# Kernel tuning notes

Measured on AMD Instinct MI355X. Metric: run time of the kernel, lower is better.

## Reference

```python
import jax, jax.numpy as jnp
import numpy as np

B, S, D, H, L, MAXSEQ = 32, 512, 768, 1024, 4, 1024


def setup_inputs() -> dict:
    key = jax.random.key(0)
    ks = jax.random.split(key, 10)
    s_in = 1.0 / np.sqrt(H)
    inp = {
        "x": jax.random.normal(ks[0], (B, S, D), dtype=jnp.float32),
        "pos_emb": jax.random.normal(ks[1], (1, MAXSEQ, D), dtype=jnp.float32),
        # layer 0 input->hidden weights (GRU: 3 gates stacked)
        "W_ih0": jax.random.uniform(ks[2], (3 * H, D), jnp.float32, -s_in, s_in),
        # layers 1..L-1 input->hidden weights
        "W_ih": jax.random.uniform(ks[3], (L - 1, 3 * H, H), jnp.float32, -s_in, s_in),
        "W_hh": jax.random.uniform(ks[4], (L, 3 * H, H), jnp.float32, -s_in, s_in),
        "b_ih": jax.random.uniform(ks[5], (L, 3 * H), jnp.float32, -s_in, s_in),
        "b_hh": jax.random.uniform(ks[6], (L, 3 * H), jnp.float32, -s_in, s_in),
        "W_out": jax.random.uniform(ks[7], (D, H), jnp.float32, -s_in, s_in),
        "b_out": jax.random.uniform(ks[8], (D,), jnp.float32, -s_in, s_in),
    }
    return inp


def _gru_cell(x, h, Wih, Whh, bih, bhh):
    # torch.nn.GRUCell math; gates stacked [r, z, n]
    gi = x @ Wih.T + bih  # [B, 3H]
    gh = h @ Whh.T + bhh  # [B, 3H]
    i_r, i_z, i_n = jnp.split(gi, 3, axis=-1)
    h_r, h_z, h_n = jnp.split(gh, 3, axis=-1)
    r = jax.nn.sigmoid(i_r + h_r)
    z = jax.nn.sigmoid(i_z + h_z)
    n = jnp.tanh(i_n + r * h_n)
    return (1.0 - z) * n + z * h


def reference(x, pos_emb, W_ih0, W_ih, W_hh, b_ih, b_hh, W_out, b_out):
    b, s, _ = x.shape
    xp = x + pos_emb[:, :s, :]          # add positional embedding
    xs = jnp.swapaxes(xp, 0, 1)         # [S, B, D] for scan over time

    def step(hs, xt):                   # hs: [L, B, H]
        inp = xt
        new_hs = []
        for l in range(L):
            Wih = W_ih0 if l == 0 else W_ih[l - 1]
            h = _gru_cell(inp, hs[l], Wih, W_hh[l], b_ih[l], b_hh[l])
            new_hs.append(h)
            inp = h
        return jnp.stack(new_hs), inp

    h0 = jnp.zeros((L, b, H), dtype=x.dtype)
    hs_final, outs = jax.lax.scan(step, h0, xs)  # outs: [S, B, H]
    out_seq = jnp.swapaxes(outs, 0, 1) @ W_out.T + b_out  # [B, S, D]
    return out_seq, hs_final
```

## Files before the change

kernel.cpp:

```cpp
#include <hip/hip_runtime.h>

#define B_ 32
#define S_ 512
#define D_ 768
#define H_ 1024
#define L_ 4
#define TH 3072
#define NPL 64
#define NITER (S_ + L_ - 1)

typedef unsigned short u16;
typedef unsigned int u32;
typedef __bf16 bf16x8 __attribute__((ext_vector_type(8)));
typedef float f32x4 __attribute__((ext_vector_type(4)));

__device__ __forceinline__ u16 f2b(float f) {
  unsigned u = __builtin_bit_cast(unsigned, f);
  u += 0x7fffu + ((u >> 16) & 1u);
  return (u16)(u >> 16);
}
__device__ __forceinline__ float b2f(u16 h) {
  return __builtin_bit_cast(float, ((unsigned)h) << 16);
}
__device__ __forceinline__ unsigned pack2(float a, float b) {
  return (unsigned)f2b(a) | ((unsigned)f2b(b) << 16);
}

__global__ __launch_bounds__(256) void cvt_kernel(const float* __restrict__ src,
                                                  u16* __restrict__ dst, int n4) {
  int i = blockIdx.x * 256 + threadIdx.x;
  int stride = gridDim.x * 256;
  for (; i < n4; i += stride) {
    float4 f = ((const float4*)src)[i];
    uint2 o;
    o.x = pack2(f.x, f.y);
    o.y = pack2(f.z, f.w);
    ((uint2*)dst)[i] = o;
  }
}

__global__ __launch_bounds__(256) void gi0_gemm(const float* __restrict__ x,
                                                const float* __restrict__ pos,
                                                const u16* __restrict__ W0,
                                                const float* __restrict__ bih0,
                                                u16* __restrict__ GI0) {
  const int n0 = blockIdx.x * 64;
  const int m0 = blockIdx.y * 64;
  __shared__ u16 sA[64 * 72];
  __shared__ u16 sB[64 * 72];
  const int tid = threadIdx.x, lane = tid & 63, wid = tid >> 6;
  const int wm = wid >> 1, wn = wid & 1;
  const int fr = lane & 15, fk = (lane >> 4) * 8;
  f32x4 acc[2][2] = {};
  for (int k0 = 0; k0 < D_; k0 += 64) {
    for (int sl = tid; sl < 512; sl += 256) {
      int r = sl >> 3, c = sl & 7;
      int m = m0 + r, si = m >> 5, b = m & 31;
      const float* xp = x + (size_t)((b << 9) + si) * D_ + k0 + c * 8;
      const float* pp = pos + (size_t)si * D_ + k0 + c * 8;
      float4 x0 = *(const float4*)xp, x1 = *(const float4*)(xp + 4);
      float4 p0 = *(const float4*)pp, p1 = *(const float4*)(pp + 4);
      uint4 o;
      o.x = pack2(x0.x + p0.x, x0.y + p0.y);
      o.y = pack2(x0.z + p0.z, x0.w + p0.w);
      o.z = pack2(x1.x + p1.x, x1.y + p1.y);
      o.w = pack2(x1.z + p1.z, x1.w + p1.w);
      *(uint4*)&sA[r * 72 + c * 8] = o;
      *(uint4*)&sB[r * 72 + c * 8] =
          *(const uint4*)(W0 + (size_t)(n0 + r) * D_ + k0 + c * 8);
    }
    __syncthreads();
#pragma unroll
    for (int kk = 0; kk < 2; ++kk) {
      bf16x8 a0 = *(const bf16x8*)&sA[(wm * 32 + fr) * 72 + kk * 32 + fk];
      bf16x8 a1 = *(const bf16x8*)&sA[(wm * 32 + 16 + fr) * 72 + kk * 32 + fk];
      bf16x8 b0 = *(const bf16x8*)&sB[(wn * 32 + fr) * 72 + kk * 32 + fk];
      bf16x8 b1 = *(const bf16x8*)&sB[(wn * 32 + 16 + fr) * 72 + kk * 32 + fk];
      acc[0][0] = __builtin_amdgcn_mfma_f32_16x16x32_bf16(a0, b0, acc[0][0], 0, 0, 0);
      acc[0][1] = __builtin_amdgcn_mfma_f32_16x16x32_bf16(a0, b1, acc[0][1], 0, 0, 0);
      acc[1][0] = __builtin_amdgcn_mfma_f32_16x16x32_bf16(a1, b0, acc[1][0], 0, 0, 0);
      acc[1][1] = __builtin_amdgcn_mfma_f32_16x16x32_bf16(a1, b1, acc[1][1], 0, 0, 0);
    }
    __syncthreads();
  }
#pragma unroll
  for (int mi = 0; mi < 2; ++mi)
#pragma unroll
    for (int ni = 0; ni < 2; ++ni)
#pragma unroll
      for (int r = 0; r < 4; ++r) {
        int m = m0 + wm * 32 + mi * 16 + (lane >> 4) * 4 + r;
        int n = n0 + wn * 32 + ni * 16 + fr;
        GI0[(size_t)m * TH + n] = f2b(acc[mi][ni][r] + bih0[n]);
      }
}

__global__ __launch_bounds__(256) void out_gemm(const u16* __restrict__ H3,
                                                const u16* __restrict__ Wo,
                                                const float* __restrict__ bo,
                                                float* __restrict__ out) {
  const int n0 = blockIdx.x * 64;
  const int m0 = blockIdx.y * 64;
  __shared__ u16 sA[64 * 72];
  __shared__ u16 sB[64 * 72];
  const int tid = threadIdx.x, lane = tid & 63, wid = tid >> 6;
  const int wm = wid >> 1, wn = wid & 1;
  const int fr = lane & 15, fk = (lane >> 4) * 8;
  f32x4 acc[2][2] = {};
  for (int k0 = 0; k0 < H_; k0 += 64) {
    for (int sl = tid; sl < 512; sl += 256) {
      int r = sl >> 3, c = sl & 7;
      int m = m0 + r, b = m >> 9, si = m & 511;
      *(uint4*)&sA[r * 72 + c * 8] =
          *(const uint4*)(H3 + (size_t)((si << 5) + b) * H_ + k0 + c * 8);
      *(uint4*)&sB[r * 72 + c * 8] =
          *(const uint4*)(Wo + (size_t)(n0 + r) * H_ + k0 + c * 8);
    }
    __syncthreads();
#pragma unroll
    for (int kk = 0; kk < 2; ++kk) {
      bf16x8 a0 = *(const bf16x8*)&sA[(wm * 32 + fr) * 72 + kk * 32 + fk];
      bf16x8 a1 = *(const bf16x8*)&sA[(wm * 32 + 16 + fr) * 72 + kk * 32 + fk];
      bf16x8 b0 = *(const bf16x8*)&sB[(wn * 32 + fr) * 72 + kk * 32 + fk];
      bf16x8 b1 = *(const bf16x8*)&sB[(wn * 32 + 16 + fr) * 72 + kk * 32 + fk];
      acc[0][0] = __builtin_amdgcn_mfma_f32_16x16x32_bf16(a0, b0, acc[0][0], 0, 0, 0);
      acc[0][1] = __builtin_amdgcn_mfma_f32_16x16x32_bf16(a0, b1, acc[0][1], 0, 0, 0);
      acc[1][0] = __builtin_amdgcn_mfma_f32_16x16x32_bf16(a1, b0, acc[1][0], 0, 0, 0);
      acc[1][1] = __builtin_amdgcn_mfma_f32_16x16x32_bf16(a1, b1, acc[1][1], 0, 0, 0);
    }
    __syncthreads();
  }
#pragma unroll
  for (int mi = 0; mi < 2; ++mi)
#pragma unroll
    for (int ni = 0; ni < 2; ++ni)
#pragma unroll
      for (int r = 0; r < 4; ++r) {
        int m = m0 + wm * 32 + mi * 16 + (lane >> 4) * 4 + r;
        int n = n0 + wn * 32 + ni * 16 + fr;
        out[(size_t)m * D_ + n] = acc[mi][ni][r] + bo[n];
      }
}

__global__ __launch_bounds__(512, 1) void rnn_persist(
    const u16* __restrict__ Whh, const u16* __restrict__ Wih,
    const u16* __restrict__ GI0, const float* __restrict__ bih,
    const float* __restrict__ bhh, u16* __restrict__ hg ,
    int* flags , u16* __restrict__ H3, float* __restrict__ hsf) {
  const int bid = blockIdx.x;
  const int l = bid >> 6;
  const int n0 = (bid & 63) << 4;
  const int tid = threadIdx.x, lane = tid & 63, wid = tid >> 6;
  const int fr = lane & 15, q = lane >> 4;

  __shared__ float red[8][3][32][20];

  bf16x8 w[3][8];
  if (l == 0) {
    const int kb = wid << 7;
#pragma unroll
    for (int g = 0; g < 3; ++g)
#pragma unroll
      for (int kt = 0; kt < 4; ++kt) {
        const u16* p = Whh + (((size_t)((g << 10) + n0 + fr)) << 10) + kb +
                       kt * 32 + q * 8;
        asm volatile("global_load_dwordx4 %0, %1, off"
                     : "=v"(w[g][kt]) : "v"(p));
      }
  } else {
    const int mat = wid >> 2;
    const u16* Wp = (mat == 0) ? (Wih + (((size_t)(l - 1) * TH) << 10))
                               : (Whh + (((size_t)l * TH) << 10));
    const int kb = (wid & 3) << 8;
#pragma unroll
    for (int g = 0; g < 3; ++g)
#pragma unroll
      for (int kt = 0; kt < 8; ++kt) {
        const u16* p = Wp + (((size_t)((g << 10) + n0 + fr)) << 10) + kb +
                       kt * 32 + q * 8;
        asm volatile("global_load_dwordx4 %0, %1, off"
                     : "=v"(w[g][kt]) : "v"(p));
      }
  }
  asm volatile("s_waitcnt vmcnt(0)" ::: "memory");

  const int* pw;
  if (l == 0) {
    pw = flags + ((0 << 6) + (wid << 3) + (lane & 7)) * 16;
  } else {
    const int srcl = (wid < 4) ? (l - 1) : l;
    pw = flags + ((srcl << 6) + ((wid & 3) << 4) + (lane & 15)) * 16;
  }
  const int* f_p1 = (l < 3) ? flags + (((l + 1) << 6) + lane) * 16
                            : flags + ((l << 6) + lane) * 16;
  int* f_mine = flags + ((l << 6) + (bid & 63)) * 16;

  const int gb = tid >> 4;
  const int jj = tid & 15;
  const int gj = n0 + jj;
  float bihv[3], bhhv[3];
#pragma unroll
  for (int g = 0; g < 3; ++g) {
    bihv[g] = (l > 0) ? bih[l * TH + (g << 10) + gj] : 0.f;
    bhhv[g] = bhh[l * TH + (g << 10) + gj];
  }
  float hpriv = 0.f;
  __syncthreads();

  for (int s = 0; s < NITER; ++s) {
    const int t = s - l;
    if (t < 0 || t >= S_) {
      if (tid == 0) {
        int v = s + 1;
        asm volatile("global_store_dword %0, %1, off sc0 sc1" ::"v"(f_mine), "v"(v)
                     : "memory");
      }
      continue;
    }
    const int prev = (s - 1) & 3;

    float gp0 = 0.f, gp1 = 0.f, gp2 = 0.f;
    if (l == 0) {
      const u16* gp = GI0 + (size_t)((t << 5) + gb) * TH + gj;
      gp0 = b2f(gp[0]);
      gp1 = b2f(gp[1024]);
      gp2 = b2f(gp[2048]);
    }

    for (;;) {
      int fv;
      asm volatile("global_load_dword %0, %1, off sc0 sc1\n\ts_waitcnt vmcnt(0)"
                   : "=v"(fv) : "v"(pw) : "memory");
      __builtin_amdgcn_sched_barrier(0);
      if (__all(fv >= s)) break;
      __builtin_amdgcn_s_sleep(1);
    }

    f32x4 acc[2][3] = {};
    if (l == 0) {
      const u16* hp = hg + (prev << 15);
      const int kb = wid << 7;
      bf16x8 afr[2][4];
#pragma unroll
      for (int mt = 0; mt < 2; ++mt)
#pragma unroll
        for (int kt = 0; kt < 4; ++kt) {
          const u16* p = hp + (((mt << 4) + fr) << 10) + kb + kt * 32 + q * 8;
          asm volatile("global_load_dwordx4 %0, %1, off sc0 sc1"
                       : "=v"(afr[mt][kt]) : "v"(p) : "memory");
        }
      asm volatile("s_waitcnt vmcnt(0)" ::: "memory");
      __builtin_amdgcn_sched_barrier(0);
#pragma unroll
      for (int kt = 0; kt < 4; ++kt)
#pragma unroll
        for (int g = 0; g < 3; ++g) {
          acc[0][g] = __builtin_amdgcn_mfma_f32_16x16x32_bf16(afr[0][kt], w[g][kt], acc[0][g], 0, 0, 0);
          acc[1][g] = __builtin_amdgcn_mfma_f32_16x16x32_bf16(afr[1][kt], w[g][kt], acc[1][g], 0, 0, 0);
        }
    } else {
      const u16* hsrc = (wid < 4) ? (hg + ((((l - 1) << 2) | prev) << 15))
                                  : (hg + (((l << 2) | prev) << 15));
      const int kb = (wid & 3) << 8;
      bf16x8 afr[2][8];
#pragma unroll
      for (int mt = 0; mt < 2; ++mt)
#pragma unroll
        for (int kt = 0; kt < 8; ++kt) {
          const u16* p = hsrc + (((mt << 4) + fr) << 10) + kb + kt * 32 + q * 8;
          asm volatile("global_load_dwordx4 %0, %1, off sc0 sc1"
                       : "=v"(afr[mt][kt]) : "v"(p) : "memory");
        }
      asm volatile("s_waitcnt vmcnt(0)" ::: "memory");
      __builtin_amdgcn_sched_barrier(0);
#pragma unroll
      for (int kt = 0; kt < 8; ++kt)
#pragma unroll
        for (int g = 0; g < 3; ++g) {
          acc[0][g] = __builtin_amdgcn_mfma_f32_16x16x32_bf16(afr[0][kt], w[g][kt], acc[0][g], 0, 0, 0);
          acc[1][g] = __builtin_amdgcn_mfma_f32_16x16x32_bf16(afr[1][kt], w[g][kt], acc[1][g], 0, 0, 0);
        }
    }

#pragma unroll
    for (int mt = 0; mt < 2; ++mt)
#pragma unroll
      for (int g = 0; g < 3; ++g)
#pragma unroll
        for (int r = 0; r < 4; ++r)
          red[wid][g][(mt << 4) + q * 4 + r][fr] = acc[mt][g][r];

    if (wid == 7) {
      const int thr = s - 2;
      for (;;) {
        int fv;
        asm volatile("global_load_dword %0, %1, off sc0 sc1\n\ts_waitcnt vmcnt(0)"
                     : "=v"(fv) : "v"(f_p1) : "memory");
        __builtin_amdgcn_sched_barrier(0);
        if (__all(fv >= thr)) break;
        __builtin_amdgcn_s_sleep(1);
      }
    }
    __syncthreads();

    float gi[3], gh[3];
#pragma unroll
    for (int g = 0; g < 3; ++g) {
      float s0 = red[0][g][gb][jj] + red[1][g][gb][jj];
      float s1 = red[2][g][gb][jj] + red[3][g][gb][jj];
      float s2 = red[4][g][gb][jj] + red[5][g][gb][jj];
      float s3 = red[6][g][gb][jj] + red[7][g][gb][jj];
      if (l == 0) {
        gh[g] = s0 + s1 + s2 + s3 + bhhv[g];
      } else {
        gi[g] = s0 + s1 + bihv[g];
        gh[g] = s2 + s3 + bhhv[g];
      }
    }
    if (l == 0) {
      gi[0] = gp0;
      gi[1] = gp1;
      gi[2] = gp2;
    }
    float rr = 1.f / (1.f + __expf(-(gi[0] + gh[0])));
    float zz = 1.f / (1.f + __expf(-(gi[1] + gh[1])));
    float xn = gi[2] + rr * gh[2];
    float nn = 1.f - 2.f / (__expf(2.f * xn) + 1.f);
    float hn = (1.f - zz) * nn + zz * hpriv;
    hpriv = hn;
    u16 hb = f2b(hn);
    u16* hd = hg + (((l << 2) | (s & 3)) << 15) + (gb << 10) + gj;
    {
      u32 hv = hb;
      asm volatile("global_store_short %0, %1, off sc0 sc1" ::"v"(hd), "v"(hv)
                   : "memory");
    }
    asm volatile("s_waitcnt vmcnt(0)" ::: "memory");
    __syncthreads();
    if (tid == 0) {
      int v = s + 1;
      asm volatile("global_store_dword %0, %1, off sc0 sc1" ::"v"(f_mine), "v"(v)
                   : "memory");
    }
    if (l == 3) H3[(((size_t)(t << 5) + gb) << 10) + gj] = hb;
    if (t == S_ - 1) hsf[((l << 5) + gb) * 1024 + gj] = hn;
  }
}

extern "C" void kernel_launch(void* const* d_in, const int* in_sizes, int n_in,
                              void* d_out, int out_size, void* d_ws, size_t ws_size,
                              hipStream_t stream) {
  const float* x = (const float*)d_in[0];
  const float* pos = (const float*)d_in[1];
  const float* Wih0 = (const float*)d_in[2];
  const float* Wih = (const float*)d_in[3];
  const float* Whh = (const float*)d_in[4];
  const float* bih = (const float*)d_in[5];
  const float* bhh = (const float*)d_in[6];
  const float* Wout = (const float*)d_in[7];
  const float* bout = (const float*)d_in[8];
  float* out = (float*)d_out;

  char* ws = (char*)d_ws;
  size_t o = 0;
  u16* wih0_b = (u16*)(ws + o); o += (size_t)TH * D_ * 2;
  u16* wih_b  = (u16*)(ws + o); o += (size_t)3 * TH * H_ * 2;
  u16* whh_b  = (u16*)(ws + o); o += (size_t)4 * TH * H_ * 2;
  u16* wout_b = (u16*)(ws + o); o += (size_t)D_ * H_ * 2;
  u16* GI0    = (u16*)(ws + o); o += (size_t)S_ * B_ * TH * 2;
  u16* H3     = (u16*)(ws + o); o += (size_t)S_ * B_ * H_ * 2;
  u16* hg     = (u16*)(ws + o); o += (size_t)L_ * 4 * B_ * H_ * 2;
  int* flags  = (int*)(ws + o); o += (size_t)L_ * 64 * 16 * 4;

  cvt_kernel<<<512, 256, 0, stream>>>(Wih0, wih0_b, TH * D_ / 4);
  cvt_kernel<<<512, 256, 0, stream>>>(Wih, wih_b, 3 * TH * H_ / 4);
  cvt_kernel<<<512, 256, 0, stream>>>(Whh, whh_b, 4 * TH * H_ / 4);
  cvt_kernel<<<512, 256, 0, stream>>>(Wout, wout_b, D_ * H_ / 4);
  hipMemsetAsync(hg, 0, (size_t)L_ * 4 * B_ * H_ * 2 + (size_t)L_ * 64 * 16 * 4,
                 stream);

  gi0_gemm<<<dim3(TH / 64, (S_ * B_) / 64), 256, 0, stream>>>(x, pos, wih0_b, bih, GI0);

  float* hsf = out + (size_t)B_ * S_ * D_;
  rnn_persist<<<256, 512, 0, stream>>>(whh_b, wih_b, GI0, bih, bhh, hg, flags, H3,
                                       hsf);

  out_gemm<<<dim3(D_ / 64, (S_ * B_) / 64), 256, 0, stream>>>(H3, wout_b, bout, out);
}
```

Measured before the change: 3.429 ms.

## Replace end-of-step block barrier with per-wave atomic flag increments and double-buffered LDS

Each wave now signals completion by atomically incrementing the block's flag after its own store drains, so the trailing __syncthreads and single-thread flag store are gone. Waiters compare against 8x the step count. The reduction scratch buffer is double-buffered by step parity in dynamic LDS, so the next step's writes cannot clobber the current step's reads without that barrier. The wait for the downstream layer (WAR on the ring buffer) moves to the start of the step. This cuts one barrier per recurrent step but adds atomic traffic and doubles the LDS footprint.

```diff
diff --git a/kernel.cpp b/kernel.cpp
--- a/kernel.cpp
+++ b/kernel.cpp
@@ -8,6 +8,7 @@
 #define TH 3072
 #define NPL 64
 #define NITER (S_ + L_ - 1)
+#define RED_LDS (2 * 8 * 3 * 32 * 20 * 4)
 
 typedef unsigned short u16;
 typedef unsigned int u32;
@@ -147,13 +148,15 @@
     const u16* __restrict__ GI0, const float* __restrict__ bih,
     const float* __restrict__ bhh, u16* __restrict__ hg ,
     int* flags , u16* __restrict__ H3, float* __restrict__ hsf) {
+  extern __shared__ float red[];
   const int bid = blockIdx.x;
   const int l = bid >> 6;
   const int n0 = (bid & 63) << 4;
   const int tid = threadIdx.x, lane = tid & 63, wid = tid >> 6;
   const int fr = lane & 15, q = lane >> 4;
 
-  __shared__ float red[8][3][32][20];
+#define RED(par, w, g, row, col) \
+  red[(((((par)*8 + (w)) * 3 + (g)) * 32 + (row)) * 20) + (col)]
 
   bf16x8 w[3][8];
   if (l == 0) {
@@ -210,14 +213,26 @@
   for (int s = 0; s < NITER; ++s) {
     const int t = s - l;
     if (t < 0 || t >= S_) {
-      if (tid == 0) {
-        int v = s + 1;
-        asm volatile("global_store_dword %0, %1, off sc0 sc1" ::"v"(f_mine), "v"(v)
-                     : "memory");
-      }
+      if (lane == 0)
+        __hip_atomic_fetch_add(f_mine, 1, __ATOMIC_RELAXED,
+                               __HIP_MEMORY_SCOPE_AGENT);
       continue;
     }
     const int prev = (s - 1) & 3;
+    const int s8 = s << 3;
+    const int par = s & 1;
+
+    if (wid == 7) {
+      const int thr = (s - 2) << 3;
+      for (;;) {
+        int fv;
+        asm volatile("global_load_dword %0, %1, off sc0 sc1\n\ts_waitcnt vmcnt(0)"
+                     : "=v"(fv) : "v"(f_p1) : "memory");
+        __builtin_amdgcn_sched_barrier(0);
+        if (__all(fv >= thr)) break;
+        __builtin_amdgcn_s_sleep(1);
+      }
+    }
 
     float gp0 = 0.f, gp1 = 0.f, gp2 = 0.f;
     if (l == 0) {
@@ -232,7 +247,7 @@
       asm volatile("global_load_dword %0, %1, off sc0 sc1\n\ts_waitcnt vmcnt(0)"
                    : "=v"(fv) : "v"(pw) : "memory");
       __builtin_amdgcn_sched_barrier(0);
-      if (__all(fv >= s)) break;
+      if (__all(fv >= s8)) break;
       __builtin_amdgcn_s_sleep(1);
     }
 
@@ -288,28 +303,16 @@
       for (int g = 0; g < 3; ++g)
 #pragma unroll
         for (int r = 0; r < 4; ++r)
-          red[wid][g][(mt << 4) + q * 4 + r][fr] = acc[mt][g][r];
-
-    if (wid == 7) {
-      const int thr = s - 2;
-      for (;;) {
-        int fv;
-        asm volatile("global_load_dword %0, %1, off sc0 sc1\n\ts_waitcnt vmcnt(0)"
-                     : "=v"(fv) : "v"(f_p1) : "memory");
-        __builtin_amdgcn_sched_barrier(0);
-        if (__all(fv >= thr)) break;
-        __builtin_amdgcn_s_sleep(1);
-      }
-    }
+          RED(par, wid, g, (mt << 4) + q * 4 + r, fr) = acc[mt][g][r];
     __syncthreads();
 
     float gi[3], gh[3];
 #pragma unroll
     for (int g = 0; g < 3; ++g) {
-      float s0 = red[0][g][gb][jj] + red[1][g][gb][jj];
-      float s1 = red[2][g][gb][jj] + red[3][g][gb][jj];
-      float s2 = red[4][g][gb][jj] + red[5][g][gb][jj];
-      float s3 = red[6][g][gb][jj] + red[7][g][gb][jj];
+      float s0 = RED(par, 0, g, gb, jj) + RED(par, 1, g, gb, jj);
+      float s1 = RED(par, 2, g, gb, jj) + RED(par, 3, g, gb, jj);
+      float s2 = RED(par, 4, g, gb, jj) + RED(par, 5, g, gb, jj);
+      float s3 = RED(par, 6, g, gb, jj) + RED(par, 7, g, gb, jj);
       if (l == 0) {
         gh[g] = s0 + s1 + s2 + s3 + bhhv[g];
       } else {
@@ -336,15 +339,13 @@
                    : "memory");
     }
     asm volatile("s_waitcnt vmcnt(0)" ::: "memory");
-    __syncthreads();
-    if (tid == 0) {
-      int v = s + 1;
-      asm volatile("global_store_dword %0, %1, off sc0 sc1" ::"v"(f_mine), "v"(v)
-                   : "memory");
-    }
+    if (lane == 0)
+      __hip_atomic_fetch_add(f_mine, 1, __ATOMIC_RELAXED,
+                             __HIP_MEMORY_SCOPE_AGENT);
     if (l == 3) H3[(((size_t)(t << 5) + gb) << 10) + gj] = hb;
     if (t == S_ - 1) hsf[((l << 5) + gb) * 1024 + gj] = hn;
   }
+#undef RED
 }
 
 extern "C" void kernel_launch(void* const* d_in, const int* in_sizes, int n_in,
@@ -382,8 +383,10 @@
   gi0_gemm<<<dim3(TH / 64, (S_ * B_) / 64), 256, 0, stream>>>(x, pos, wih0_b, bih, GI0);
 
   float* hsf = out + (size_t)B_ * S_ * D_;
-  rnn_persist<<<256, 512, 0, stream>>>(whh_b, wih_b, GI0, bih, bhh, hg, flags, H3,
-                                       hsf);
+  hipFuncSetAttribute((const void*)rnn_persist,
+                      hipFuncAttributeMaxDynamicSharedMemorySize, RED_LDS);
+  rnn_persist<<<256, 512, RED_LDS, stream>>>(whh_b, wih_b, GI0, bih, bhh, hg,
+                                             flags, H3, hsf);
 
   out_gemm<<<dim3(D_ / 64, (S_ * B_) / 64), 256, 0, stream>>>(H3, wout_b, bout, out);
 }
```

Measured after the change: 4.549 ms. +32.7%, slower.
